# Kernel tuning notes

Measured on AMD Instinct MI355X. Metric: run time of the kernel, lower is better.

Reference implementation:

```python
import jax, jax.numpy as jnp
import numpy as np

MAX_DIST = 32.0
GRID_RES = 0.5
BOX = int(np.ceil(2 * MAX_DIST / GRID_RES + 1))  # 129


def setup_inputs() -> dict:
    key = jax.random.key(0)
    k1, k2 = jax.random.split(key)
    B, N, F = 1, 500000, 32
    # scale so most points are inside the [-32, 32] box, some outside
    coords = jax.random.normal(k1, (B, N, 3), dtype=jnp.float32) * 20.0
    features = jax.random.normal(k2, (B, N, F), dtype=jnp.float32)
    return {"coords": coords, "features": features}


def reference(coords, features):
    B, N, _ = coords.shape
    F = features.shape[2]
    # voxel indices
    gc = jnp.round((coords + MAX_DIST) / GRID_RES).astype(jnp.int32)  # (B,N,3)
    in_box = jnp.all((gc >= 0) & (gc < BOX), axis=-1)                 # (B,N)
    # instead of boolean_mask (dynamic shape), zero out-of-box features and
    # clamp their indices; scatter-add of zeros is a no-op, matching
    # tf.scatter_nd's duplicate-summing semantics on the masked set.
    feats = jnp.where(in_box[..., None], features, jnp.zeros((), features.dtype))
    gcc = jnp.clip(gc, 0, BOX - 1)
    b_idx = jnp.broadcast_to(jnp.arange(B)[:, None], (B, N))
    grid = jnp.zeros((B, BOX, BOX, BOX, F), dtype=features.dtype)
    grid = grid.at[b_idx, gcc[..., 0], gcc[..., 1], gcc[..., 2]].add(feats)
    return grid
```

## Files before the change

### kernel.cpp

```cpp
#include <hip/hip_runtime.h>
#include <hip/hip_bf16.h>

#define MAX_DIST 32.0f
#define BOX 129
#define BOX3 (129 * 129 * 129)

__global__ void __launch_bounds__(256) build_lists_kernel(
    const float* __restrict__ coords,
    int* __restrict__ head,
    int* __restrict__ next,
    int N) {
  int stride = gridDim.x * blockDim.x;
  for (int p = blockIdx.x * blockDim.x + threadIdx.x; p < N; p += stride) {
    float x = coords[3 * p + 0];
    float y = coords[3 * p + 1];
    float z = coords[3 * p + 2];
    int gx = __float2int_rn((x + MAX_DIST) * 2.0f);
    int gy = __float2int_rn((y + MAX_DIST) * 2.0f);
    int gz = __float2int_rn((z + MAX_DIST) * 2.0f);
    if ((unsigned)gx < BOX && (unsigned)gy < BOX && (unsigned)gz < BOX) {
      int cell = (gx * BOX + gy) * BOX + gz;
      next[p] = atomicExch(&head[cell], p);
    }
  }
}

__global__ void __launch_bounds__(256) gather_kernel(
    const int* __restrict__ head,
    const int* __restrict__ next,
    const float4* __restrict__ feats4,
    float4* __restrict__ grid4) {
  long t = (long)blockIdx.x * blockDim.x + threadIdx.x;
  if (t >= (long)BOX3 * 8) return;
  int cell = (int)(t >> 3);
  int fp = (int)(t & 7);
  float4 acc = make_float4(0.f, 0.f, 0.f, 0.f);
  int p = head[cell];
  while (p >= 0) {
    float4 v = feats4[(long)p * 8 + fp];
    acc.x += v.x; acc.y += v.y; acc.z += v.z; acc.w += v.w;
    p = next[p];
  }
  grid4[t] = acc;
}

__global__ void __launch_bounds__(256) scatter_fallback_kernel(
    const float* __restrict__ coords,
    const float2* __restrict__ feats,
    float* __restrict__ grid,
    int N) {
  int total = N * 16;
  int stride = gridDim.x * blockDim.x;
  for (int t = blockIdx.x * blockDim.x + threadIdx.x; t < total; t += stride) {
    int p = t >> 4;
    int fp = t & 15;
    float x = coords[3 * p + 0];
    float y = coords[3 * p + 1];
    float z = coords[3 * p + 2];
    int gx = __float2int_rn((x + MAX_DIST) * 2.0f);
    int gy = __float2int_rn((y + MAX_DIST) * 2.0f);
    int gz = __float2int_rn((z + MAX_DIST) * 2.0f);
    if ((unsigned)gx < BOX && (unsigned)gy < BOX && (unsigned)gz < BOX) {
      float2 v = feats[(long)p * 16 + fp];
      long base = (((long)gx * BOX + gy) * BOX + gz) * 32 + 2 * fp;
      atomicAdd(&grid[base + 0], v.x);
      atomicAdd(&grid[base + 1], v.y);
    }
  }
}

extern "C" void kernel_launch(void* const* d_in, const int* in_sizes, int n_in,
                              void* d_out, int out_size, void* d_ws, size_t ws_size,
                              hipStream_t stream) {
  const float* coords = (const float*)d_in[0];
  int N = in_sizes[0] / 3;

  size_t head_bytes = (size_t)BOX3 * sizeof(int);
  size_t head_pad   = (head_bytes + 255) & ~(size_t)255;
  size_t needed     = head_pad + (size_t)N * sizeof(int);

  if (ws_size >= needed) {
    int* head = (int*)d_ws;
    int* next = (int*)((char*)d_ws + head_pad);

    hipMemsetAsync(head, 0xFF, head_bytes, stream);

    int blocks2 = (N + 255) / 256;
    build_lists_kernel<<<blocks2, 256, 0, stream>>>(coords, head, next, N);

    long total3 = (long)BOX3 * 8;
    int blocks3 = (int)((total3 + 255) / 256);
    gather_kernel<<<blocks3, 256, 0, stream>>>(
        head, next, (const float4*)d_in[1], (float4*)d_out);
  } else {
    hipMemsetAsync(d_out, 0, (size_t)out_size * sizeof(float), stream);
    int total = N * 16;
    int blocks = 4096;
    if (blocks > (total + 255) / 256) blocks = (total + 255) / 256;
    scatter_fallback_kernel<<<blocks, 256, 0, stream>>>(
        coords, (const float2*)d_in[1], (float*)d_out, N);
  }
}
```

Measured before the change: 374.2 us.

## Gather only occupied voxels via worklist and memset output

The list-building pass now records each cell the first time it becomes non-empty, by appending it to a worklist with a global atomic counter. The gather kernel is a grid-stride loop over worklist entries only, and the output grid is zeroed with a memset instead of having every cell written by the gather. This removes the head reads and empty-cell threads across the roughly 2.1M-cell grid, in exchange for a global atomic per occupied cell, a full memset of the 275MB output, and scattered rather than coalesced output writes.

Result: slower. 437.9 us (+17.0%).

```diff
diff --git a/kernel.cpp b/kernel.cpp
--- a/kernel.cpp
+++ b/kernel.cpp
@@ -9,6 +9,8 @@
     const float* __restrict__ coords,
     int* __restrict__ head,
     int* __restrict__ next,
+    int* __restrict__ wl,
+    int* __restrict__ wl_cnt,
     int N) {
   int stride = gridDim.x * blockDim.x;
   for (int p = blockIdx.x * blockDim.x + threadIdx.x; p < N; p += stride) {
@@ -20,28 +22,37 @@
     int gz = __float2int_rn((z + MAX_DIST) * 2.0f);
     if ((unsigned)gx < BOX && (unsigned)gy < BOX && (unsigned)gz < BOX) {
       int cell = (gx * BOX + gy) * BOX + gz;
-      next[p] = atomicExch(&head[cell], p);
+      int old = atomicExch(&head[cell], p);
+      next[p] = old;
+      if (old < 0) {
+        int s = atomicAdd(wl_cnt, 1);
+        wl[s] = cell;
+      }
     }
   }
 }
 
-__global__ void __launch_bounds__(256) gather_kernel(
+__global__ void __launch_bounds__(256) gather_wl_kernel(
     const int* __restrict__ head,
     const int* __restrict__ next,
+    const int* __restrict__ wl,
+    const int* __restrict__ wl_cnt,
     const float4* __restrict__ feats4,
     float4* __restrict__ grid4) {
-  long t = (long)blockIdx.x * blockDim.x + threadIdx.x;
-  if (t >= (long)BOX3 * 8) return;
-  int cell = (int)(t >> 3);
-  int fp = (int)(t & 7);
-  float4 acc = make_float4(0.f, 0.f, 0.f, 0.f);
-  int p = head[cell];
-  while (p >= 0) {
-    float4 v = feats4[(long)p * 8 + fp];
-    acc.x += v.x; acc.y += v.y; acc.z += v.z; acc.w += v.w;
-    p = next[p];
+  int cnt = *wl_cnt;
+  long total = (long)cnt * 8;
+  long stride = (long)gridDim.x * blockDim.x;
+  for (long t = (long)blockIdx.x * blockDim.x + threadIdx.x; t < total; t += stride) {
+    int wi = (int)(t >> 3);
+    int fp = (int)(t & 7);
+    int cell = wl[wi];
+    float4 acc = make_float4(0.f, 0.f, 0.f, 0.f);
+    for (int p = head[cell]; p >= 0; p = next[p]) {
+      float4 v = feats4[(long)p * 8 + fp];
+      acc.x += v.x; acc.y += v.y; acc.z += v.z; acc.w += v.w;
+    }
+    grid4[(long)cell * 8 + fp] = acc;
   }
-  grid4[t] = acc;
 }
 
 __global__ void __launch_bounds__(256) scatter_fallback_kernel(
@@ -69,29 +80,35 @@
   }
 }
 
+static inline size_t pad256(size_t x) { return (x + 255) & ~(size_t)255; }
+
 extern "C" void kernel_launch(void* const* d_in, const int* in_sizes, int n_in,
                               void* d_out, int out_size, void* d_ws, size_t ws_size,
                               hipStream_t stream) {
   const float* coords = (const float*)d_in[0];
   int N = in_sizes[0] / 3;
 
-  size_t head_bytes = (size_t)BOX3 * sizeof(int);
-  size_t head_pad   = (head_bytes + 255) & ~(size_t)255;
-  size_t needed     = head_pad + (size_t)N * sizeof(int);
+  size_t head_b = pad256((size_t)BOX3 * sizeof(int));
+  size_t next_b = pad256((size_t)N * sizeof(int));
+  size_t cnt_b  = 256;
+  size_t wl_b   = pad256((size_t)BOX3 * sizeof(int));
+  size_t needed = head_b + next_b + cnt_b + wl_b;
 
   if (ws_size >= needed) {
-    int* head = (int*)d_ws;
-    int* next = (int*)((char*)d_ws + head_pad);
+    int* head   = (int*)d_ws;
+    int* next   = (int*)((char*)d_ws + head_b);
+    int* wl_cnt = (int*)((char*)d_ws + head_b + next_b);
+    int* wl     = (int*)((char*)d_ws + head_b + next_b + cnt_b);
 
-    hipMemsetAsync(head, 0xFF, head_bytes, stream);
+    hipMemsetAsync(head, 0xFF, (size_t)BOX3 * sizeof(int), stream);
+    hipMemsetAsync(wl_cnt, 0, sizeof(int), stream);
+    hipMemsetAsync(d_out, 0, (size_t)out_size * sizeof(float), stream);
 
     int blocks2 = (N + 255) / 256;
-    build_lists_kernel<<<blocks2, 256, 0, stream>>>(coords, head, next, N);
+    build_lists_kernel<<<blocks2, 256, 0, stream>>>(coords, head, next, wl, wl_cnt, N);
 
-    long total3 = (long)BOX3 * 8;
-    int blocks3 = (int)((total3 + 255) / 256);
-    gather_kernel<<<blocks3, 256, 0, stream>>>(
-        head, next, (const float4*)d_in[1], (float4*)d_out);
+    gather_wl_kernel<<<4096, 256, 0, stream>>>(
+        head, next, wl, wl_cnt, (const float4*)d_in[1], (float4*)d_out);
   } else {
     hipMemsetAsync(d_out, 0, (size_t)out_size * sizeof(float), stream);
     int total = N * 16;
```
